# Optimization experiments

Measured on AMD Instinct MI355X. Metric: run time of the kernel, lower is better.

## Reference

```python
import jax, jax.numpy as jnp
import numpy as np

IN_CH = 8      # in_channels
CIN = 80       # cin_channels (mel)
DI_BASE = 2
POS_GROUP = 4
NCH = 256      # n_channels
NLAYERS = 8
K = 3          # kernel_size
B = 1          # spect batch; audio batch = B * POS_GROUP
T = 4096
C2L = 2 * NCH * NLAYERS


def _conv1x1(x, w, b):
    # x: [B, C, T], w: [O, C], b: [O]
    return jnp.einsum('bct,oc->bot', x, w) + b[None, :, None]


def _dilated_conv(x, w, b, dilation):
    # x: [B, C, T], w: [O, C, K], 'same' padding as in torch Conv1d
    pad = dilation * (K - 1) // 2
    y = jax.lax.conv_general_dilated(
        x, w, window_strides=(1,), padding=[(pad, pad)],
        rhs_dilation=(dilation,), dimension_numbers=('NCH', 'OIH', 'NCH'))
    return y + b[None, :, None]


def setup_inputs() -> dict:
    key = jax.random.key(0)
    ks = jax.random.split(key, 12)
    s = 0.05
    d = {}
    d['audio'] = jax.random.normal(ks[0], (B * POS_GROUP, IN_CH, T), jnp.float32)
    d['spect'] = jax.random.normal(ks[1], (B, CIN, T), jnp.float32)
    d['pos'] = jax.random.randint(ks[2], (B * POS_GROUP,), 0, POS_GROUP)
    d['start_w'] = jax.random.normal(ks[3], (NCH, IN_CH), jnp.float32) * s
    d['start_b'] = jnp.zeros((NCH,), jnp.float32)
    d['cond_w'] = jax.random.normal(ks[4], (C2L, CIN), jnp.float32) * s
    d['cond_b'] = jnp.zeros((C2L,), jnp.float32)
    d['pos_emb_w'] = jax.random.normal(ks[5], (POS_GROUP, 128), jnp.float32) * s
    d['pos_lin_w'] = jax.random.normal(ks[6], (C2L, 128), jnp.float32) * s
    d['pos_lin_b'] = jnp.zeros((C2L,), jnp.float32)
    d['in_w'] = jax.random.normal(ks[7], (NLAYERS, 2 * NCH, NCH, K), jnp.float32) * s
    d['in_b'] = jnp.zeros((NLAYERS, 2 * NCH), jnp.float32)
    d['rs_w'] = jax.random.normal(ks[8], (NLAYERS - 1, 2 * NCH, NCH), jnp.float32) * s
    d['rs_b'] = jnp.zeros((NLAYERS - 1, 2 * NCH), jnp.float32)
    d['rs_last_w'] = jax.random.normal(ks[9], (NCH, NCH), jnp.float32) * s
    d['rs_last_b'] = jnp.zeros((NCH,), jnp.float32)
    d['end_w'] = jax.random.normal(ks[10], (2 * IN_CH, NCH), jnp.float32) * s
    d['end_b'] = jnp.zeros((2 * IN_CH,), jnp.float32)
    return d


def reference(audio, spect, pos, start_w, start_b, cond_w, cond_b,
              pos_emb_w, pos_lin_w, pos_lin_b, in_w, in_b,
              rs_w, rs_b, rs_last_w, rs_last_b, end_w, end_b):
    h = _conv1x1(audio, start_w, start_b)               # [BG, NCH, T]
    out = jnp.zeros_like(h)
    cond = _conv1x1(spect, cond_w, cond_b)              # [B, 2*NCH*L, T]
    # repeat(1, pos_group, 1).view(-1, C, T) == consecutive batch tiling
    cond = jnp.repeat(cond, POS_GROUP, axis=0)          # [BG, 2*NCH*L, T]
    pe = jax.nn.relu(pos_emb_w[pos])                    # [BG, 128]
    pc = (pe @ pos_lin_w.T + pos_lin_b)[:, :, None]     # [BG, 2*NCH*L, 1]
    for i in range(NLAYERS):
        off = i * 2 * NCH
        in_act = (_dilated_conv(h, in_w[i], in_b[i], DI_BASE ** i)
                  + cond[:, off:off + 2 * NCH]
                  + pc[:, off:off + 2 * NCH])
        acts = jnp.tanh(in_act[:, :NCH]) * jax.nn.sigmoid(in_act[:, NCH:])
        if i < NLAYERS - 1:
            rs = _conv1x1(acts, rs_w[i], rs_b[i])       # [BG, 2*NCH, T]
            h = h + rs[:, :NCH]
            out = out + rs[:, NCH:]
        else:
            out = out + _conv1x1(acts, rs_last_w, rs_last_b)
    y = _conv1x1(out, end_w, end_b)                     # [BG, 2*IN_CH, T]
    return y[:, :IN_CH], y[:, IN_CH:]
```

## Files before the change

kernel.cpp:

```cpp
#include <hip/hip_runtime.h>
#include <stdint.h>

#define T_LEN 4096
#define PAD   128
#define HROWS (T_LEN + 2*PAD)
#define NCH   256
#define M2    512
#define BG    4
#define NL    8

using f4  = __attribute__((ext_vector_type(4))) float;
using bh8 = __attribute__((ext_vector_type(8))) short;
using s4v = __attribute__((ext_vector_type(4))) short;
using u4  = __attribute__((ext_vector_type(4))) unsigned int;

static __device__ __forceinline__ short f2b(float f){
  unsigned u = __builtin_bit_cast(unsigned, f);
  unsigned r = (u + 0x7FFFu + ((u >> 16) & 1u)) >> 16;
  return (short)r;
}
static __device__ __forceinline__ float b2f(short s){
  unsigned u = ((unsigned)(unsigned short)s) << 16;
  return __builtin_bit_cast(float, u);
}

#define MFMA(a,b,c) __builtin_amdgcn_mfma_f32_16x16x32_bf16((a),(b),(c),0,0,0)


#define PAD_BLK0 1024
#define E_BLK0   1280
#define ST_BLK0  1408
#define CB_BLK0  1536
#define H0_BLK0  1600
#define ALL_BLKS 1856

__global__ __launch_bounds__(256) void prep_all(
    const float* __restrict__ audio, const float* __restrict__ spect,
    const int* __restrict__ pos, const float* __restrict__ start_w,
    const float* __restrict__ start_b, const float* __restrict__ cond_w,
    const float* __restrict__ cond_b, const float* __restrict__ pos_emb_w,
    const float* __restrict__ pos_lin_w, const float* __restrict__ pos_lin_b,
    const float* __restrict__ in_w, const float* __restrict__ in_b,
    const float* __restrict__ rs_w, const float* __restrict__ rs_b,
    const float* __restrict__ rs_last_w, const float* __restrict__ rs_last_b,
    const float* __restrict__ end_w, const float* __restrict__ end_b,
    short* __restrict__ W1, short* __restrict__ W2, short* __restrict__ Wcn,
    float* __restrict__ rsb8, short* __restrict__ hA, short* __restrict__ hB,
    short* __restrict__ Es, float* __restrict__ ebl, short* __restrict__ spectT,
    float* __restrict__ cb){
  __shared__ float smem[4224];
  const int bid = blockIdx.x, tid = threadIdx.x;

  if (bid < PAD_BLK0){
    const int G1 = NL*3*8*8*4*64;
    const int G2 = NL*8*8*2*64;
    const int G4 = NL*8*4*4*64;
    const int n3 = NL*M2;
    for (int q = bid*256 + tid; q < G1+G2+G4+n3; q += 1024*256){
      if (q < G1){
        int lane = q & 63, f = (q >> 6) & 3, kk = (q >> 8) & 7, w = (q >> 11) & 7;
        int lt = q >> 14;
        int tap = lt % 3, l = lt / 3;
        int o = (f < 2) ? (w*32 + f*16 + (lane & 15)) : (256 + w*32 + (f-2)*16 + (lane & 15));
        int c0 = kk*32 + (lane >> 4)*8;
        const float* src = in_w + (((size_t)(l*M2 + o)*NCH + c0)*3) + tap;
        bh8 pk;
        #pragma unroll
        for (int j = 0; j < 8; ++j) pk[j] = f2b(src[j*3]);
        *(bh8*)(W1 + (size_t)q*8) = pk;
      } else if (q < G1+G2){
        int p = q - G1;
        int lane = p & 63, f = (p >> 6) & 1, kk = (p >> 7) & 7, w = (p >> 10) & 7;
        int l = p >> 13;
        int o = w*32 + f*16 + (lane & 15);
        int c0 = kk*32 + (lane >> 4)*8;
        bh8 pk;
        if (l < 7){
          const f4* s = (const f4*)(rs_w + ((size_t)(l*M2 + o))*NCH + c0);
          f4 a = s[0], bvv = s[1];
          #pragma unroll
          for (int j = 0; j < 4; ++j){ pk[j] = f2b(a[j]); pk[4+j] = f2b(bvv[j]); }
        } else {
          #pragma unroll
          for (int j = 0; j < 8; ++j) pk[j] = 0;
        }
        *(bh8*)(W2 + (size_t)p*8) = pk;
      } else if (q < G1+G2+G4){
        int p = q - G1 - G2;
        int lane = p & 63, f = (p >> 6) & 3, kk = (p >> 8) & 3, w = (p >> 10) & 7;
        int l = p >> 13;
        int o = (f < 2) ? (w*32 + f*16 + (lane & 15)) : (256 + w*32 + (f-2)*16 + (lane & 15));
        int k0 = kk*32 + (lane >> 4)*8;
        bh8 pk;
        if (k0 < 80){
          const f4* s = (const f4*)(cond_w + (size_t)(l*M2 + o)*80 + k0);
          f4 a = s[0], bvv = s[1];
          #pragma unroll
          for (int j = 0; j < 4; ++j){ pk[j] = f2b(a[j]); pk[4+j] = f2b(bvv[j]); }
        } else {
          #pragma unroll
          for (int j = 0; j < 8; ++j) pk[j] = 0;
        }
        *(bh8*)(Wcn + (size_t)p*8) = pk;
      } else {
        int k = q - G1 - G2 - G4;
        int o = k & 511, l = k >> 9;
        rsb8[k] = (l < 7) ? rs_b[l*M2 + o] : 0.f;
      }
    }
  } else if (bid < E_BLK0){
    int i = (bid - PAD_BLK0)*256 + tid;
    short* h = (i < 32768) ? hA : hB;
    int j = (i & 32767) << 3;
    int b = j >> 16;
    int r = j & 65535;
    int row = r >> 8, c = r & 255;
    int grow = (row < PAD) ? row : (T_LEN + PAD + (row - PAD));
    *(u4*)(h + ((size_t)b*HROWS + grow)*NCH + c) = (u4){0,0,0,0};
  } else if (bid < ST_BLK0){
    float* ew_s = smem; float* red = smem + 256;
    int e = bid - E_BLK0;
    const int l = e >> 4, o = e & 15;
    const int c = tid;
    ew_s[c] = end_w[o*256 + c];
    __syncthreads();
    const float* Wsrc = (l < 7) ? (rs_w + ((size_t)(l*M2 + NCH))*NCH) : rs_last_w;
    float acc = 0.f;
    #pragma unroll 8
    for (int cp = 0; cp < 256; ++cp)
      acc += ew_s[cp] * Wsrc[(size_t)cp*NCH + c];
    int kk = c >> 5, g = (c >> 3) & 3, j = c & 7;
    Es[(((size_t)l*8 + kk)*64 + g*16 + o)*8 + j] = f2b(acc);
    float bv = (l < 7) ? rs_b[l*M2 + NCH + c] : rs_last_b[c];
    red[c] = ew_s[c] * bv;
    __syncthreads();
    for (int s = 128; s > 0; s >>= 1){
      if (c < s) red[c] += red[c + s];
      __syncthreads();
    }
    if (c == 0) ebl[l*16 + o] = red[0] + ((l == 0) ? end_b[o] : 0.f);
  } else if (bid < CB_BLK0){
    float (*tile)[65] = (float(*)[65])smem;
    int e = bid - ST_BLK0;
    int t0 = (e & 63)*64, k0 = (e >> 6)*64;
    for (int i = tid; i < 64*64; i += 256){
      int kr = i >> 6, tt = i & 63;
      int k = k0 + kr;
      tile[kr][tt] = (k < 80) ? spect[(size_t)k*T_LEN + t0 + tt] : 0.f;
    }
    __syncthreads();
    for (int i = tid; i < 64*64; i += 256){
      int r = i >> 6, kk = i & 63;
      spectT[(size_t)(t0 + r)*128 + k0 + kk] = f2b(tile[kk][r]);
    }
  } else if (bid < H0_BLK0){
    int e = bid - CB_BLK0;
    int b = e >> 4;
    int ch = (e & 15)*256 + tid;
    int p = pos[b];
    float acc = pos_lin_b[ch] + in_b[ch] + cond_b[ch];
    for (int k = 0; k < 128; ++k){
      float ev = pos_emb_w[p*128 + k];
      ev = ev > 0.f ? ev : 0.f;
      acc += ev * pos_lin_w[ch*128 + k];
    }
    cb[b*4096 + ch] = acc;
  } else {
    float* sw = smem; float* sb = smem + 2048;
    int e = bid - H0_BLK0;
    int b = e >> 6, t0 = (e & 63)*64;
    for (int i = tid; i < NCH*8; i += 256) sw[i] = start_w[i];
    for (int i = tid; i < NCH;   i += 256) sb[i] = start_b[i];
    __syncthreads();
    int t = t0 + (tid & 63);
    int cg = tid >> 6;
    float av[8];
    #pragma unroll
    for (int ic = 0; ic < 8; ++ic) av[ic] = audio[((size_t)(b*8 + ic))*T_LEN + t];
    short* dst = hA + ((size_t)b*HROWS + PAD + t)*NCH;
    for (int c = cg*64; c < cg*64 + 64; ++c){
      float acc = sb[c];
      #pragma unroll
      for (int ic = 0; ic < 8; ++ic) acc += sw[c*8 + ic]*av[ic];
      dst[c] = f2b(acc);
    }
  }
}

template<int DIL>
__global__ __launch_bounds__(512, 2) void wn_layer(
    const short* __restrict__ hSrc, short* __restrict__ hDst,
    const short* __restrict__ W1l, const short* __restrict__ W2l,
    const short* __restrict__ Wcl, const short* __restrict__ Esl,
    const short* __restrict__ spectTp,
    const float* __restrict__ cb_l, const float* __restrict__ rsb_l,
    const float* __restrict__ ebl_l, float* __restrict__ yacc,
    int flags){

  __shared__ short Ht[192*NCH];
  __shared__ short xb[64*NCH];
  __shared__ short St[64*128];

  constexpr int tbR   = (DIL <= 64) ? DIL : 64;
  constexpr int WROWS = (DIL <= 64) ? (64 + 2*DIL) : 192;

  const int tid  = threadIdx.x;
  const int w    = tid >> 6, lane = tid & 63;
  const int l15  = lane & 15, g = lane >> 4;
  const int lin  = blockIdx.x + (blockIdx.y << 6);
  const int nl2  = ((lin & 7) << 5) + (lin >> 3);
  const int tile = nl2 & 63, b = nl2 >> 6;
  const int sw8  = (l15 & 7) << 3;
  const bool first = flags & 1, last = flags & 2;

  f4 acc[4][4];
  #pragma unroll
  for (int f = 0; f < 4; ++f)
    #pragma unroll
    for (int nf = 0; nf < 4; ++nf) acc[f][nf] = (f4){0.f,0.f,0.f,0.f};

  bh8 Ap[4][4], Bp[3][4];

#define LAc(S, BUF) do{ const short* _p = Wcl + w*8192 + (S)*2048 + lane*8; \
    Ap[BUF][0]=*(const bh8*)(_p);      Ap[BUF][1]=*(const bh8*)(_p+512); \
    Ap[BUF][2]=*(const bh8*)(_p+1024); Ap[BUF][3]=*(const bh8*)(_p+1536); }while(0)
#define LBc(S, BUF) do{ const int _c=((S)*32+g*8)^sw8; \
    Bp[BUF][0]=*(const bh8*)(St + ( 0+l15)*128 + _c); \
    Bp[BUF][1]=*(const bh8*)(St + (16+l15)*128 + _c); \
    Bp[BUF][2]=*(const bh8*)(St + (32+l15)*128 + _c); \
    Bp[BUF][3]=*(const bh8*)(St + (48+l15)*128 + _c); }while(0)
#define LA1(S, BUF) do{ const int _tap=(S)>>3, _kk=(S)&7; \
    const short* _p = W1l + _tap*131072 + w*16384 + _kk*2048 + lane*8; \
    Ap[BUF][0]=*(const bh8*)(_p);      Ap[BUF][1]=*(const bh8*)(_p+512); \
    Ap[BUF][2]=*(const bh8*)(_p+1024); Ap[BUF][3]=*(const bh8*)(_p+1536); }while(0)
#define LB1(S, BUF) do{ const int _tap=(S)>>3, _kk=(S)&7; \
    const int _tb=_tap*tbR; const int _sw=(((_tb+l15)&7)<<3); \
    const short* _hb = Ht + (_tb+l15)*NCH + ((_kk*32+g*8)^_sw); \
    Bp[BUF][0]=*(const bh8*)(_hb); \
    Bp[BUF][1]=*(const bh8*)(_hb + 16*NCH); \
    Bp[BUF][2]=*(const bh8*)(_hb + 32*NCH); \
    Bp[BUF][3]=*(const bh8*)(_hb + 48*NCH); }while(0)
#define LAX(S, BUF) do{ if((S)<3) LAc((S),BUF); else LA1((S)-3,BUF); }while(0)
#define LBX(S, BUF) do{ if((S)<3) LBc((S),BUF); else LB1((S)-3,BUF); }while(0)
#define LA2(S, BUF) do{ \
    const short* _p = W2l + w*8192 + (S)*1024 + lane*8; \
    Ap[BUF][0]=*(const bh8*)(_p);      Ap[BUF][1]=*(const bh8*)(_p+512); }while(0)
#define LB2(S, BUF) do{ const int _c=((S)*32+g*8)^sw8; \
    Bp[BUF][0]=*(const bh8*)(xb + ( 0+l15)*NCH + _c); \
    Bp[BUF][1]=*(const bh8*)(xb + (16+l15)*NCH + _c); \
    Bp[BUF][2]=*(const bh8*)(xb + (32+l15)*NCH + _c); \
    Bp[BUF][3]=*(const bh8*)(xb + (48+l15)*NCH + _c); }while(0)

  LAX(0, 0);

  {
    constexpr int NCHUNK = WROWS*32;
    constexpr int KITER  = (NCHUNK + 511)/512;
    #pragma unroll
    for (int k = 0; k < KITER; ++k){
      int i = tid + k*512;
      if (NCHUNK % 512 == 0 || i < NCHUNK){
        int r = i >> 5, c16 = (i & 31) << 3;
        int grow = (DIL <= 64) ? (tile*64 - DIL + r)
                               : (tile*64 + ((r >> 6) - 1)*128 + (r & 63));
        u4 v = *(const u4*)(hSrc + ((size_t)(b*HROWS + PAD + grow))*NCH + c16);
        *(u4*)(Ht + r*NCH + (c16 ^ ((r & 7) << 3))) = v;
      }
    }
    #pragma unroll
    for (int s = 0; s < 2; ++s){
      int id = tid + s*512;
      int r = id >> 4, c8 = (id & 15) << 3;
      u4 v = *(const u4*)(spectTp + (size_t)(tile*64 + r)*128 + c8);
      *(u4*)(St + r*128 + (c8 ^ ((r & 7) << 3))) = v;
    }
  }
  LAX(1, 1);
  __syncthreads();

  LBX(0, 0);
  LAX(2, 2);
  LBX(1, 1);
  #pragma unroll
  for (int s = 0; s < 27; ++s){
    const int curA = s & 3, curB = s % 3;
    if (s < 24) LAX(s+3, (s+3) & 3);
    if (s < 25) LBX(s+2, (s+2) % 3);
    #pragma unroll
    for (int f = 0; f < 4; ++f)
      #pragma unroll
      for (int nf = 0; nf < 4; ++nf)
        acc[f][nf] = MFMA(Ap[curA][f], Bp[curB][nf], acc[f][nf]);
  }

  float bias[4][4];
  #pragma unroll
  for (int f = 0; f < 4; ++f){
    int ch = ((f < 2) ? (w*32 + f*16) : (256 + w*32 + (f-2)*16)) + 4*g;
    f4 t = *(const f4*)(cb_l + b*4096 + ch);
    #pragma unroll
    for (int j = 0; j < 4; ++j) bias[f][j] = t[j];
  }
  float rbv[2][4];
  #pragma unroll
  for (int f = 0; f < 2; ++f){
    f4 t = *(const f4*)(rsb_l + w*32 + f*16 + 4*g);
    #pragma unroll
    for (int j = 0; j < 4; ++j) rbv[f][j] = t[j];
  }

  #pragma unroll
  for (int f = 0; f < 2; ++f){
    #pragma unroll
    for (int nf = 0; nf < 4; ++nf){
      int tl = nf*16 + l15;
      s4v pk;
      #pragma unroll
      for (int j = 0; j < 4; ++j){
        float xl = acc[f][nf][j]   + bias[f][j];
        float xh = acc[f+2][nf][j] + bias[f+2][j];
        xl = fminf(fmaxf(xl, -30.f), 30.f);
        xh = fminf(fmaxf(xh, -30.f), 30.f);
        float e2 = __expf(2.f*xl);
        float th = (e2 - 1.f)/(e2 + 1.f);
        float sg = 1.f/(1.f + __expf(-xh));
        pk[j] = f2b(th * sg);
      }
      *(s4v*)(xb + tl*NCH + ((w*32 + f*16 + 4*g) ^ sw8)) = pk;
    }
  }
  if (!last){ LA2(0, 0); LA2(1, 1); }
  __syncthreads();

  if (!last){
    #pragma unroll
    for (int f = 0; f < 2; ++f)
      #pragma unroll
      for (int nf = 0; nf < 4; ++nf) acc[f][nf] = (f4){0.f,0.f,0.f,0.f};
    LB2(0, 0);
    #pragma unroll
    for (int s = 0; s < 8; ++s){
      const int curA = s % 3, curB = s & 1;
      if (s < 6) LA2(s+2, (s+2) % 3);
      if (s < 7) LB2(s+1, curB ^ 1);
      #pragma unroll
      for (int f = 0; f < 2; ++f)
        #pragma unroll
        for (int nf = 0; nf < 4; ++nf)
          acc[f][nf] = MFMA(Ap[curA][f], Bp[curB][nf], acc[f][nf]);
    }
    constexpr int swcBase = tbR & 7;
    const int swc = (((swcBase + l15) & 7) << 3);
    #pragma unroll
    for (int f = 0; f < 2; ++f){
      #pragma unroll
      for (int nf = 0; nf < 4; ++nf){
        int tl = nf*16 + l15;
        int cb0 = w*32 + f*16 + 4*g;
        s4v hold = *(const s4v*)(Ht + (tbR + tl)*NCH + (cb0 ^ swc));
        s4v pk;
        #pragma unroll
        for (int j = 0; j < 4; ++j)
          pk[j] = f2b(b2f(hold[j]) + acc[f][nf][j] + rbv[f][j]);
        *(s4v*)(hDst + ((size_t)b*HROWS + PAD + tile*64 + tl)*NCH + cb0) = pk;
      }
    }
  }
  {
    const int nfq = w & 3, kh = w >> 2;
    f4 ya = (f4){0.f,0.f,0.f,0.f};
    #pragma unroll
    for (int s = 0; s < 4; ++s){
      int kks = kh*4 + s;
      bh8 av = *(const bh8*)(Esl + ((size_t)kks*64 + lane)*8);
      bh8 bv = *(const bh8*)(xb + (nfq*16 + l15)*NCH + ((kks*32 + g*8) ^ sw8));
      ya = MFMA(av, bv, ya);
    }
    float* yp = yacc + (((size_t)(b*T_LEN + tile*64 + nfq*16 + l15))*2 + kh)*16 + g*4;
    f4 prev = first ? (f4){0.f,0.f,0.f,0.f} : *(const f4*)yp;
    f4 o;
    #pragma unroll
    for (int j = 0; j < 4; ++j)
      o[j] = prev[j] + ya[j] + ((kh == 0) ? ebl_l[g*4 + j] : 0.f);
    *(f4*)yp = o;
  }
#undef LAc
#undef LBc
#undef LA1
#undef LB1
#undef LAX
#undef LBX
#undef LA2
#undef LB2
}

__global__ void final_y(const float* __restrict__ yacc, float* __restrict__ y){
  __shared__ float tl[16][65];
  int b = blockIdx.y, t0 = blockIdx.x*64;
  int i = threadIdx.x;
  #pragma unroll
  for (int s = 0; s < 4; ++s){
    int idx = i + s*256;
    int t = idx >> 4, o = idx & 15;
    size_t base = ((size_t)(b*T_LEN + t0 + t))*32 + o;
    tl[o][t] = yacc[base] + yacc[base + 16];
  }
  __syncthreads();
  #pragma unroll
  for (int s = 0; s < 4; ++s){
    int idx = i + s*256;
    int o = idx >> 6, t = idx & 63;
    float v = tl[o][t];
    float* dst = (o < 8) ? (y + ((size_t)(b*8 + o))*T_LEN)
                         : (y + 131072 + ((size_t)(b*8 + o - 8))*T_LEN);
    dst[t0 + t] = v;
  }
}

extern "C" void kernel_launch(void* const* d_in, const int* in_sizes, int n_in,
                              void* d_out, int out_size, void* d_ws, size_t ws_size,
                              hipStream_t stream){
  const float* audio      = (const float*)d_in[0];
  const float* spect      = (const float*)d_in[1];
  const int*   pos        = (const int*)  d_in[2];
  const float* start_w    = (const float*)d_in[3];
  const float* start_b    = (const float*)d_in[4];
  const float* cond_w     = (const float*)d_in[5];
  const float* cond_b     = (const float*)d_in[6];
  const float* pos_emb_w  = (const float*)d_in[7];
  const float* pos_lin_w  = (const float*)d_in[8];
  const float* pos_lin_b  = (const float*)d_in[9];
  const float* in_w       = (const float*)d_in[10];
  const float* in_b       = (const float*)d_in[11];
  const float* rs_w       = (const float*)d_in[12];
  const float* rs_b       = (const float*)d_in[13];
  const float* rs_last_w  = (const float*)d_in[14];
  const float* rs_last_b  = (const float*)d_in[15];
  const float* end_w      = (const float*)d_in[16];
  const float* end_b      = (const float*)d_in[17];
  float* y = (float*)d_out;

  char* ws = (char*)d_ws;
  size_t off = 0;
  auto alloc = [&](size_t bytes) -> void* {
    void* p = ws + off;
    off += (bytes + 255) & ~(size_t)255;
    return p;
  };
  const size_t hBytes = (size_t)BG*HROWS*NCH*2;
  short* hA     = (short*)alloc(hBytes);
  short* hB     = (short*)alloc(hBytes);
  short* W1     = (short*)alloc((size_t)NL*3*8*8*4*512*2);
  short* W2     = (short*)alloc((size_t)NL*8*8*2*512*2);
  short* Wcn    = (short*)alloc((size_t)NL*8*4*4*512*2);
  float* rsb8   = (float*)alloc((size_t)NL*M2*4);
  float* cb     = (float*)alloc((size_t)BG*4096*4);
  short* spectT = (short*)alloc((size_t)4096*128*2);
  short* Es     = (short*)alloc((size_t)NL*8*64*8*2);
  float* ebl    = (float*)alloc((size_t)NL*16*4);
  float* yacc   = (float*)alloc((size_t)BG*T_LEN*2*16*4);
  if (off > ws_size) return;

  prep_all<<<ALL_BLKS, 256, 0, stream>>>(
      audio, spect, pos, start_w, start_b, cond_w, cond_b, pos_emb_w, pos_lin_w,
      pos_lin_b, in_w, in_b, rs_w, rs_b, rs_last_w, rs_last_b, end_w, end_b,
      W1, W2, Wcn, rsb8, hA, hB, Es, ebl, spectT, cb);

  for (int l = 0; l < NL; ++l){
    const short* hS = (l & 1) ? hB : hA;
    short*       hD = (l & 1) ? hA : hB;
    int flags = (l == 0 ? 1 : 0) | (l == NL-1 ? 2 : 0);
    const short* W1p = W1 + (size_t)l*3*131072;
    const short* W2p = W2 + (size_t)l*65536;
    const short* Wcp = Wcn + (size_t)l*65536;
    const short* Esp = Es + (size_t)l*4096;
    const float* cbp = cb + l*M2;
    const float* rbp = rsb8 + l*M2;
    const float* ebp = ebl + l*16;
    dim3 grid(64, BG);
    switch (l){
      case 0: wn_layer<  1><<<grid, 512, 0, stream>>>(hS, hD, W1p, W2p, Wcp, Esp, spectT, cbp, rbp, ebp, yacc, flags); break;
      case 1: wn_layer<  2><<<grid, 512, 0, stream>>>(hS, hD, W1p, W2p, Wcp, Esp, spectT, cbp, rbp, ebp, yacc, flags); break;
      case 2: wn_layer<  4><<<grid, 512, 0, stream>>>(hS, hD, W1p, W2p, Wcp, Esp, spectT, cbp, rbp, ebp, yacc, flags); break;
      case 3: wn_layer<  8><<<grid, 512, 0, stream>>>(hS, hD, W1p, W2p, Wcp, Esp, spectT, cbp, rbp, ebp, yacc, flags); break;
      case 4: wn_layer< 16><<<grid, 512, 0, stream>>>(hS, hD, W1p, W2p, Wcp, Esp, spectT, cbp, rbp, ebp, yacc, flags); break;
      case 5: wn_layer< 32><<<grid, 512, 0, stream>>>(hS, hD, W1p, W2p, Wcp, Esp, spectT, cbp, rbp, ebp, yacc, flags); break;
      case 6: wn_layer< 64><<<grid, 512, 0, stream>>>(hS, hD, W1p, W2p, Wcp, Esp, spectT, cbp, rbp, ebp, yacc, flags); break;
      case 7: wn_layer<128><<<grid, 512, 0, stream>>>(hS, hD, W1p, W2p, Wcp, Esp, spectT, cbp, rbp, ebp, yacc, flags); break;
    }
  }
  final_y<<<dim3(64, BG), 256, 0, stream>>>(yacc, y);
}
```

Measured before the change: 229.9 us.

## Stage h and spect tiles via global_load_lds and shorten weight prefetch depth

Replaces the register round-trip staging of the h and spectrogram tiles into shared memory with direct global-to-LDS loads. The XOR swizzle moves from the LDS destination address to the global source address. The A-operand prefetch depth in both GEMM loops is reduced: the layer conv drops from four register buffers to three shared with B, and the residual GEMM from three to two. This frees VGPRs and cuts staging instructions, but exposes more weight-load latency to the MFMA chain.

New measurement: 230.1 us. Within noise of the previous version (+0.1%).

```diff
diff --git a/kernel.cpp b/kernel.cpp
--- a/kernel.cpp
+++ b/kernel.cpp
@@ -219,7 +219,7 @@
     #pragma unroll
     for (int nf = 0; nf < 4; ++nf) acc[f][nf] = (f4){0.f,0.f,0.f,0.f};
 
-  bh8 Ap[4][4], Bp[3][4];
+  bh8 Ap[3][4], Bp[3][4];
 
 #define LAc(S, BUF) do{ const short* _p = Wcl + w*8192 + (S)*2048 + lane*8; \
     Ap[BUF][0]=*(const bh8*)(_p);      Ap[BUF][1]=*(const bh8*)(_p+512); \
@@ -254,43 +254,48 @@
   LAX(0, 0);
 
   {
-    constexpr int NCHUNK = WROWS*32;
-    constexpr int KITER  = (NCHUNK + 511)/512;
-    #pragma unroll
-    for (int k = 0; k < KITER; ++k){
-      int i = tid + k*512;
-      if (NCHUNK % 512 == 0 || i < NCHUNK){
-        int r = i >> 5, c16 = (i & 31) << 3;
+    constexpr int SEGS = WROWS/2;
+    #pragma unroll
+    for (int k = 0; k < (SEGS + 7)/8; ++k){
+      int seg = w + k*8;
+      if (SEGS % 8 == 0 || seg < SEGS){
+        int r = seg*2 + (lane >> 5);
         int grow = (DIL <= 64) ? (tile*64 - DIL + r)
                                : (tile*64 + ((r >> 6) - 1)*128 + (r & 63));
-        u4 v = *(const u4*)(hSrc + ((size_t)(b*HROWS + PAD + grow))*NCH + c16);
-        *(u4*)(Ht + r*NCH + (c16 ^ ((r & 7) << 3))) = v;
+        int cb = ((lane & 31) << 4) ^ ((r & 7) << 4);
+        const short* gp = hSrc + ((size_t)(b*HROWS + PAD + grow))*NCH + (cb >> 1);
+        __builtin_amdgcn_global_load_lds(
+            (const __attribute__((address_space(1))) unsigned int*)gp,
+            (__attribute__((address_space(3))) unsigned int*)(Ht + seg*512),
+            16, 0, 0);
       }
     }
     #pragma unroll
-    for (int s = 0; s < 2; ++s){
-      int id = tid + s*512;
-      int r = id >> 4, c8 = (id & 15) << 3;
-      u4 v = *(const u4*)(spectTp + (size_t)(tile*64 + r)*128 + c8);
-      *(u4*)(St + r*128 + (c8 ^ ((r & 7) << 3))) = v;
+    for (int k = 0; k < 2; ++k){
+      int seg = w + k*8;
+      int r = seg*4 + (lane >> 4);
+      int cb = ((lane & 15) << 4) ^ ((r & 7) << 4);
+      const short* gp = spectTp + (size_t)(tile*64 + r)*128 + (cb >> 1);
+      __builtin_amdgcn_global_load_lds(
+          (const __attribute__((address_space(1))) unsigned int*)gp,
+          (__attribute__((address_space(3))) unsigned int*)(St + seg*512),
+          16, 0, 0);
     }
   }
   LAX(1, 1);
   __syncthreads();
 
   LBX(0, 0);
-  LAX(2, 2);
   LBX(1, 1);
   #pragma unroll
   for (int s = 0; s < 27; ++s){
-    const int curA = s & 3, curB = s % 3;
-    if (s < 24) LAX(s+3, (s+3) & 3);
-    if (s < 25) LBX(s+2, (s+2) % 3);
+    const int cur = s % 3, pf = (s+2) % 3;
+    if (s < 25){ LAX(s+2, pf); LBX(s+2, pf); }
     #pragma unroll
     for (int f = 0; f < 4; ++f)
       #pragma unroll
       for (int nf = 0; nf < 4; ++nf)
-        acc[f][nf] = MFMA(Ap[curA][f], Bp[curB][nf], acc[f][nf]);
+        acc[f][nf] = MFMA(Ap[cur][f], Bp[cur][nf], acc[f][nf]);
   }
 
   float bias[4][4];
@@ -329,7 +334,7 @@
       *(s4v*)(xb + tl*NCH + ((w*32 + f*16 + 4*g) ^ sw8)) = pk;
     }
   }
-  if (!last){ LA2(0, 0); LA2(1, 1); }
+  if (!last) LA2(0, 0);
   __syncthreads();
 
   if (!last){
@@ -340,14 +345,13 @@
     LB2(0, 0);
     #pragma unroll
     for (int s = 0; s < 8; ++s){
-      const int curA = s % 3, curB = s & 1;
-      if (s < 6) LA2(s+2, (s+2) % 3);
-      if (s < 7) LB2(s+1, curB ^ 1);
+      const int cur = s & 1, nxt = cur ^ 1;
+      if (s < 7){ LA2(s+1, nxt); LB2(s+1, nxt); }
       #pragma unroll
       for (int f = 0; f < 2; ++f)
         #pragma unroll
         for (int nf = 0; nf < 4; ++nf)
-          acc[f][nf] = MFMA(Ap[curA][f], Bp[curB][nf], acc[f][nf]);
+          acc[f][nf] = MFMA(Ap[cur][f], Bp[cur][nf], acc[f][nf]);
     }
     constexpr int swcBase = tbR & 7;
     const int swc = (((swcBase + l15) & 7) << 3);
```

## Overlap h-window staging with cond GEMM using direct global spect fragments

Applied to the files above, without the earlier changes.

The layer kernel no longer stages spect into shared memory. The three cond-GEMM k-steps now read B fragments straight from global memory, and their MFMAs run while the h-window global loads are still in flight in registers. The h rows are written to LDS only after those MFMAs finish. Shared Ht is sized per dilation to shrink LDS use, and the A/B register buffers are reduced to a 3-deep and 2-deep prefetch ring. The trade-offs are higher register pressure from holding the h loads in registers, uncoalesced spect fragment loads, and shallower prefetch in the residual GEMM.

After: 280.6 us. 1.22x slower.

```diff
diff --git a/kernel.cpp b/kernel.cpp
--- a/kernel.cpp
+++ b/kernel.cpp
@@ -197,12 +197,11 @@
     const float* __restrict__ ebl_l, float* __restrict__ yacc,
     int flags){
 
-  __shared__ short Ht[192*NCH];
-  __shared__ short xb[64*NCH];
-  __shared__ short St[64*128];
-
   constexpr int tbR   = (DIL <= 64) ? DIL : 64;
   constexpr int WROWS = (DIL <= 64) ? (64 + 2*DIL) : 192;
+
+  __shared__ short Ht[WROWS*NCH];
+  __shared__ short xb[64*NCH];
 
   const int tid  = threadIdx.x;
   const int w    = tid >> 6, lane = tid & 63;
@@ -219,16 +218,16 @@
     #pragma unroll
     for (int nf = 0; nf < 4; ++nf) acc[f][nf] = (f4){0.f,0.f,0.f,0.f};
 
-  bh8 Ap[4][4], Bp[3][4];
+  bh8 Ap[3][4], Bp[3][4];
 
 #define LAc(S, BUF) do{ const short* _p = Wcl + w*8192 + (S)*2048 + lane*8; \
     Ap[BUF][0]=*(const bh8*)(_p);      Ap[BUF][1]=*(const bh8*)(_p+512); \
     Ap[BUF][2]=*(const bh8*)(_p+1024); Ap[BUF][3]=*(const bh8*)(_p+1536); }while(0)
-#define LBc(S, BUF) do{ const int _c=((S)*32+g*8)^sw8; \
-    Bp[BUF][0]=*(const bh8*)(St + ( 0+l15)*128 + _c); \
-    Bp[BUF][1]=*(const bh8*)(St + (16+l15)*128 + _c); \
-    Bp[BUF][2]=*(const bh8*)(St + (32+l15)*128 + _c); \
-    Bp[BUF][3]=*(const bh8*)(St + (48+l15)*128 + _c); }while(0)
+#define LBG(S, BUF) do{ const short* _sp = spectTp + (size_t)(tile*64)*128 + (S)*32 + g*8; \
+    Bp[BUF][0]=*(const bh8*)(_sp + ( 0+l15)*128); \
+    Bp[BUF][1]=*(const bh8*)(_sp + (16+l15)*128); \
+    Bp[BUF][2]=*(const bh8*)(_sp + (32+l15)*128); \
+    Bp[BUF][3]=*(const bh8*)(_sp + (48+l15)*128); }while(0)
 #define LA1(S, BUF) do{ const int _tap=(S)>>3, _kk=(S)&7; \
     const short* _p = W1l + _tap*131072 + w*16384 + _kk*2048 + lane*8; \
     Ap[BUF][0]=*(const bh8*)(_p);      Ap[BUF][1]=*(const bh8*)(_p+512); \
@@ -240,8 +239,6 @@
     Bp[BUF][1]=*(const bh8*)(_hb + 16*NCH); \
     Bp[BUF][2]=*(const bh8*)(_hb + 32*NCH); \
     Bp[BUF][3]=*(const bh8*)(_hb + 48*NCH); }while(0)
-#define LAX(S, BUF) do{ if((S)<3) LAc((S),BUF); else LA1((S)-3,BUF); }while(0)
-#define LBX(S, BUF) do{ if((S)<3) LBc((S),BUF); else LB1((S)-3,BUF); }while(0)
 #define LA2(S, BUF) do{ \
     const short* _p = W2l + w*8192 + (S)*1024 + lane*8; \
     Ap[BUF][0]=*(const bh8*)(_p);      Ap[BUF][1]=*(const bh8*)(_p+512); }while(0)
@@ -251,46 +248,70 @@
     Bp[BUF][2]=*(const bh8*)(xb + (32+l15)*NCH + _c); \
     Bp[BUF][3]=*(const bh8*)(xb + (48+l15)*NCH + _c); }while(0)
 
-  LAX(0, 0);
+  LAc(0, 0); LAc(1, 1);
+
+  constexpr int NCHUNK = WROWS*32;
+  constexpr int KITER  = (NCHUNK + 511)/512;
+  u4 hv[KITER];
+  #pragma unroll
+  for (int k = 0; k < KITER; ++k){
+    int i = tid + k*512;
+    if (NCHUNK % 512 == 0 || i < NCHUNK){
+      int r = i >> 5, c16 = (i & 31) << 3;
+      int grow = (DIL <= 64) ? (tile*64 - DIL + r)
+                             : (tile*64 + ((r >> 6) - 1)*128 + (r & 63));
+      hv[k] = *(const u4*)(hSrc + ((size_t)(b*HROWS + PAD + grow))*NCH + c16);
+    }
+  }
+
+  LBG(0, 0); LBG(1, 1);
 
   {
-    constexpr int NCHUNK = WROWS*32;
-    constexpr int KITER  = (NCHUNK + 511)/512;
-    #pragma unroll
-    for (int k = 0; k < KITER; ++k){
-      int i = tid + k*512;
-      if (NCHUNK % 512 == 0 || i < NCHUNK){
-        int r = i >> 5, c16 = (i & 31) << 3;
-        int grow = (DIL <= 64) ? (tile*64 - DIL + r)
-                               : (tile*64 + ((r >> 6) - 1)*128 + (r & 63));
-        u4 v = *(const u4*)(hSrc + ((size_t)(b*HROWS + PAD + grow))*NCH + c16);
-        *(u4*)(Ht + r*NCH + (c16 ^ ((r & 7) << 3))) = v;
-      }
-    }
-    #pragma unroll
-    for (int s = 0; s < 2; ++s){
-      int id = tid + s*512;
-      int r = id >> 4, c8 = (id & 15) << 3;
-      u4 v = *(const u4*)(spectTp + (size_t)(tile*64 + r)*128 + c8);
-      *(u4*)(St + r*128 + (c8 ^ ((r & 7) << 3))) = v;
-    }
-  }
-  LAX(1, 1);
+    LAc(2, 2); LBG(2, 2);
+    #pragma unroll
+    for (int f = 0; f < 4; ++f)
+      #pragma unroll
+      for (int nf = 0; nf < 4; ++nf)
+        acc[f][nf] = MFMA(Ap[0][f], Bp[0][nf], acc[f][nf]);
+  }
+  {
+    LA1(0, 0);
+    #pragma unroll
+    for (int f = 0; f < 4; ++f)
+      #pragma unroll
+      for (int nf = 0; nf < 4; ++nf)
+        acc[f][nf] = MFMA(Ap[1][f], Bp[1][nf], acc[f][nf]);
+  }
+  {
+    LA1(1, 1);
+    #pragma unroll
+    for (int f = 0; f < 4; ++f)
+      #pragma unroll
+      for (int nf = 0; nf < 4; ++nf)
+        acc[f][nf] = MFMA(Ap[2][f], Bp[2][nf], acc[f][nf]);
+  }
+
+  #pragma unroll
+  for (int k = 0; k < KITER; ++k){
+    int i = tid + k*512;
+    if (NCHUNK % 512 == 0 || i < NCHUNK){
+      int r = i >> 5, c16 = (i & 31) << 3;
+      *(u4*)(Ht + r*NCH + (c16 ^ ((r & 7) << 3))) = hv[k];
+    }
+  }
   __syncthreads();
 
-  LBX(0, 0);
-  LAX(2, 2);
-  LBX(1, 1);
-  #pragma unroll
-  for (int s = 0; s < 27; ++s){
-    const int curA = s & 3, curB = s % 3;
-    if (s < 24) LAX(s+3, (s+3) & 3);
-    if (s < 25) LBX(s+2, (s+2) % 3);
+  LB1(0, 0);
+  LB1(1, 1);
+  #pragma unroll
+  for (int s = 0; s < 24; ++s){
+    const int cur = s % 3, pf = (s+2) % 3;
+    if (s < 22){ LA1(s+2, pf); LB1(s+2, pf); }
     #pragma unroll
     for (int f = 0; f < 4; ++f)
       #pragma unroll
       for (int nf = 0; nf < 4; ++nf)
-        acc[f][nf] = MFMA(Ap[curA][f], Bp[curB][nf], acc[f][nf]);
+        acc[f][nf] = MFMA(Ap[cur][f], Bp[cur][nf], acc[f][nf]);
   }
 
   float bias[4][4];
@@ -329,7 +350,7 @@
       *(s4v*)(xb + tl*NCH + ((w*32 + f*16 + 4*g) ^ sw8)) = pk;
     }
   }
-  if (!last){ LA2(0, 0); LA2(1, 1); }
+  if (!last) LA2(0, 0);
   __syncthreads();
 
   if (!last){
@@ -340,14 +361,13 @@
     LB2(0, 0);
     #pragma unroll
     for (int s = 0; s < 8; ++s){
-      const int curA = s % 3, curB = s & 1;
-      if (s < 6) LA2(s+2, (s+2) % 3);
-      if (s < 7) LB2(s+1, curB ^ 1);
+      const int cur = s & 1, nxt = cur ^ 1;
+      if (s < 7){ LA2(s+1, nxt); LB2(s+1, nxt); }
       #pragma unroll
       for (int f = 0; f < 2; ++f)
         #pragma unroll
         for (int nf = 0; nf < 4; ++nf)
-          acc[f][nf] = MFMA(Ap[curA][f], Bp[curB][nf], acc[f][nf]);
+          acc[f][nf] = MFMA(Ap[cur][f], Bp[cur][nf], acc[f][nf]);
     }
     constexpr int swcBase = tbR & 7;
     const int swc = (((swcBase + l15) & 7) << 3);
@@ -385,11 +405,9 @@
     *(f4*)yp = o;
   }
 #undef LAc
-#undef LBc
+#undef LBG
 #undef LA1
 #undef LB1
-#undef LAX
-#undef LBX
 #undef LA2
 #undef LB2
 }
```
